# Kernel tuning notes

Hardware: AMD Instinct MI355X
Metric: run time of the kernel (lower is better)

The kernel has to match this reference:

```python
import jax, jax.numpy as jnp
import numpy as np

B = 128          # batch
DIM_CODES = 256  # codes per sample
EMB = 16         # embedding dim per code
BOOK = 1024      # codebook entries per code position
Z = 512          # latent dim
NPSEUDO = 16     # pseudo inputs (VampPrior)
WDIM = DIM_CODES * EMB  # 4096


def setup_inputs() -> dict:
    key = jax.random.key(0)
    k0, k1, k2, k3, k4 = jax.random.split(key, 5)
    s = 0.02
    return {
        "w_q": jax.random.normal(k0, (B, WDIM), jnp.float32),
        "pseudo_inputs": jax.random.normal(k1, (NPSEUDO, EMB, DIM_CODES), jnp.float32),
        "W_enc": jax.random.normal(k2, (EMB * DIM_CODES, 2 * Z), jnp.float32) * s,
        "b_enc": jnp.zeros((2 * Z,), jnp.float32),
        "W_dec": jax.random.normal(k3, (Z, WDIM), jnp.float32) * s,
        "b_dec": jnp.zeros((WDIM,), jnp.float32),
        "codebook": jax.random.normal(k4, (DIM_CODES, BOOK, EMB), jnp.float32),
    }


def _dist(w_recon, codebook):
    # pykeops_square_distance: per-code squared L2 distance to all book entries
    x = w_recon.reshape(-1, DIM_CODES, EMB)              # (B, dc, e)
    x2 = jnp.sum(x * x, axis=-1)                         # (B, dc)
    c2 = jnp.sum(codebook * codebook, axis=-1)           # (dc, book)
    cross = jnp.einsum('bde,dke->bdk', x, codebook)      # (B, dc, book)
    d = x2[:, :, None] - 2.0 * cross + c2[None, :, :]    # (B, dc, book)
    idx = jnp.argmin(d, axis=2)[..., None]               # (B, dc, 1)
    return d, idx


def reference(w_q, pseudo_inputs, W_enc, b_enc, W_dec, b_dec, codebook):
    # encode: reshape w_q to (B, emb, dim_codes), append pseudo inputs
    x = jnp.swapaxes(w_q.reshape(-1, DIM_CODES, EMB), 1, 2)   # (B, e, dc)
    x = jnp.concatenate([x, pseudo_inputs], axis=0)           # (B+P, e, dc)
    h = x.reshape(x.shape[0], -1) @ W_enc + b_enc             # (B+P, 2Z)
    batch = h[:-NPSEUDO]                                      # drop pseudo rows
    mu, log_var = jnp.split(batch, 2, axis=1)                 # (B, Z) each
    z = mu                                                    # eval mode: gaussian_sample returns mu
    # decode
    w_recon = z @ W_dec + b_dec                               # (B, WDIM)
    cb = jax.lax.stop_gradient(codebook)                      # codebook.detach()
    w_dist, idx = _dist(w_recon, cb)
    return (w_dist, idx, w_recon, mu, log_var)
```

## Files before the change

### kernel.cpp

```cpp
#include <hip/hip_runtime.h>

#define OFF_WDIST 0
#define OFF_IDX   33554432
#define OFF_WREC  33587200
#define OFF_MU    34111488
#define OFF_LV    34177024

__device__ __forceinline__ float dot16(const float4* a, const float4* b) {
    float s = 0.f;
#pragma unroll
    for (int i = 0; i < 4; ++i) {
        s = fmaf(a[i].x, b[i].x, s);
        s = fmaf(a[i].y, b[i].y, s);
        s = fmaf(a[i].z, b[i].z, s);
        s = fmaf(a[i].w, b[i].w, s);
    }
    return s;
}

__global__ __launch_bounds__(256) void enc_gemm1_kernel(const float* __restrict__ w_q,
                                                        const float* __restrict__ W_enc,
                                                        float* __restrict__ part) {
    __shared__ float xs_t[64 * 128];
    __shared__ float ws[64 * 128];
    const int tid = threadIdx.x;
    const int jt = blockIdx.x & 7;
    const int kc = blockIdx.x >> 3;

    {
        const int b = tid >> 1;
        const int half = tid & 1;
        const float* src = w_q + b * 4096 + kc * 64;
#pragma unroll
        for (int u = 0; u < 8; ++u) {
            const int l0 = half * 32 + u * 4;
            const float4 v = *(const float4*)(src + l0);
            xs_t[(l0 + 0) * 128 + b] = v.x;
            xs_t[(l0 + 1) * 128 + b] = v.y;
            xs_t[(l0 + 2) * 128 + b] = v.z;
            xs_t[(l0 + 3) * 128 + b] = v.w;
        }
    }
    {
        const int l = tid >> 2;
        const int q = tid & 3;
        const int gi = (l & 15) * 256 + kc * 4 + (l >> 4);
        const float* src = W_enc + (size_t)gi * 1024 + jt * 128 + q * 32;
        float* dst = &ws[l * 128 + q * 32];
#pragma unroll
        for (int u = 0; u < 8; ++u) {
            *(float4*)(dst + u * 4) = *(const float4*)(src + u * 4);
        }
    }
    __syncthreads();

    const int tx = tid & 15;
    const int ty = tid >> 4;
    float acc[8][8];
#pragma unroll
    for (int r = 0; r < 8; ++r)
#pragma unroll
        for (int c = 0; c < 8; ++c) acc[r][c] = 0.f;

    for (int l = 0; l < 64; ++l) {
        const float4 a0 = *(const float4*)&xs_t[l * 128 + ty * 8];
        const float4 a1 = *(const float4*)&xs_t[l * 128 + ty * 8 + 4];
        const float4 w0 = *(const float4*)&ws[l * 128 + tx * 4];
        const float4 w1 = *(const float4*)&ws[l * 128 + 64 + tx * 4];
        const float av[8] = {a0.x, a0.y, a0.z, a0.w, a1.x, a1.y, a1.z, a1.w};
        const float wv[8] = {w0.x, w0.y, w0.z, w0.w, w1.x, w1.y, w1.z, w1.w};
#pragma unroll
        for (int r = 0; r < 8; ++r)
#pragma unroll
            for (int c = 0; c < 8; ++c)
                acc[r][c] = fmaf(av[r], wv[c], acc[r][c]);
    }

#pragma unroll
    for (int r = 0; r < 8; ++r) {
        const int brow = ty * 8 + r;
        float* dst = part + (size_t)(kc * 128 + brow) * 1024 + jt * 128;
        *(float4*)(dst + tx * 4)      = make_float4(acc[r][0], acc[r][1], acc[r][2], acc[r][3]);
        *(float4*)(dst + 64 + tx * 4) = make_float4(acc[r][4], acc[r][5], acc[r][6], acc[r][7]);
    }
}

__global__ __launch_bounds__(256) void enc_reduce_kernel(const float* __restrict__ part,
                                                         const float* __restrict__ b_enc,
                                                         float* __restrict__ mu_out,
                                                         float* __restrict__ lv_out) {
    const int g = blockIdx.x * 256 + threadIdx.x;
    const int b = g >> 10;
    const int j = g & 1023;
    float sum = b_enc[j];
#pragma unroll 8
    for (int kc = 0; kc < 64; ++kc) {
        sum += part[(size_t)((kc * 128 + b) << 10) + j];
    }
    if (j < 512) mu_out[b * 512 + j] = sum;
    else         lv_out[b * 512 + (j - 512)] = sum;
}

__global__ __launch_bounds__(256) void dec_gemm1_kernel(const float* __restrict__ mu_in,
                                                        const float* __restrict__ W_dec,
                                                        float* __restrict__ part) {
    __shared__ float xs_t[32 * 128];
    __shared__ float ws[32 * 128];
    const int tid = threadIdx.x;
    const int ct = blockIdx.x & 31;
    const int kc = blockIdx.x >> 5;

    {
        const int b = tid >> 1;
        const int half = tid & 1;
        const float* src = mu_in + b * 512 + kc * 32;
#pragma unroll
        for (int u = 0; u < 4; ++u) {
            const int l0 = half * 16 + u * 4;
            const float4 v = *(const float4*)(src + l0);
            xs_t[(l0 + 0) * 128 + b] = v.x;
            xs_t[(l0 + 1) * 128 + b] = v.y;
            xs_t[(l0 + 2) * 128 + b] = v.z;
            xs_t[(l0 + 3) * 128 + b] = v.w;
        }
    }
    {
        const int l = tid >> 3;
        const int q = tid & 7;
        const float* src = W_dec + (size_t)(kc * 32 + l) * 4096 + ct * 128 + q * 16;
        float* dst = &ws[l * 128 + q * 16];
#pragma unroll
        for (int u = 0; u < 4; ++u) {
            *(float4*)(dst + u * 4) = *(const float4*)(src + u * 4);
        }
    }
    __syncthreads();

    const int tx = tid & 15;
    const int ty = tid >> 4;
    float acc[8][8];
#pragma unroll
    for (int r = 0; r < 8; ++r)
#pragma unroll
        for (int c = 0; c < 8; ++c) acc[r][c] = 0.f;

    for (int l = 0; l < 32; ++l) {
        const float4 a0 = *(const float4*)&xs_t[l * 128 + ty * 8];
        const float4 a1 = *(const float4*)&xs_t[l * 128 + ty * 8 + 4];
        const float4 w0 = *(const float4*)&ws[l * 128 + tx * 4];
        const float4 w1 = *(const float4*)&ws[l * 128 + 64 + tx * 4];
        const float av[8] = {a0.x, a0.y, a0.z, a0.w, a1.x, a1.y, a1.z, a1.w};
        const float wv[8] = {w0.x, w0.y, w0.z, w0.w, w1.x, w1.y, w1.z, w1.w};
#pragma unroll
        for (int r = 0; r < 8; ++r)
#pragma unroll
            for (int c = 0; c < 8; ++c)
                acc[r][c] = fmaf(av[r], wv[c], acc[r][c]);
    }

#pragma unroll
    for (int r = 0; r < 8; ++r) {
        const int brow = ty * 8 + r;
        float* dst = part + (size_t)(kc * 128 + brow) * 4096 + ct * 128;
        *(float4*)(dst + tx * 4)      = make_float4(acc[r][0], acc[r][1], acc[r][2], acc[r][3]);
        *(float4*)(dst + 64 + tx * 4) = make_float4(acc[r][4], acc[r][5], acc[r][6], acc[r][7]);
    }
}

__global__ __launch_bounds__(256) void dec_reduce_kernel(const float* __restrict__ part,
                                                         const float* __restrict__ b_dec,
                                                         float* __restrict__ wrec_out) {
    const int g = blockIdx.x * 256 + threadIdx.x;
    const int b = g >> 12;
    const int n = g & 4095;
    float sum = b_dec[n];
#pragma unroll
    for (int kc = 0; kc < 16; ++kc) {
        sum += part[(size_t)((kc * 128 + b) << 12) + n];
    }
    wrec_out[b * 4096 + n] = sum;
}

__global__ __launch_bounds__(256) void dist_kernel(const float* __restrict__ wrec,
                                                   const float* __restrict__ cbk,
                                                   float* __restrict__ wdist,
                                                   float* __restrict__ idx_out) {
    const int dc = blockIdx.x & 255;
    const int bg = blockIdx.x >> 8;
    const int t = threadIdx.x;

    float4 xr[8][4];
    float x2[8];
#pragma unroll
    for (int r = 0; r < 8; ++r) {
        const float4* p = (const float4*)(wrec + (bg * 8 + r) * 4096 + dc * 16);
        xr[r][0] = p[0]; xr[r][1] = p[1]; xr[r][2] = p[2]; xr[r][3] = p[3];
        x2[r] = dot16(xr[r], xr[r]);
    }

    const float* cbp = cbk + (size_t)dc * 1024 * 16;
    float dv[8][4];
    float minv[8];
    int mink[8];
#pragma unroll
    for (int r = 0; r < 8; ++r) { minv[r] = 3.4e38f; mink[r] = 0; }

    const int k0 = t * 4;
#pragma unroll
    for (int kk = 0; kk < 4; ++kk) {
        const int k = k0 + kk;
        const float4* cp = (const float4*)(cbp + (size_t)k * 16);
        float4 cv[4];
        cv[0] = cp[0]; cv[1] = cp[1]; cv[2] = cp[2]; cv[3] = cp[3];
        const float cc = dot16(cv, cv);
#pragma unroll
        for (int r = 0; r < 8; ++r) {
            const float cr = dot16(xr[r], cv);
            const float dd = (x2[r] - 2.f * cr) + cc;
            dv[r][kk] = dd;
            if (dd < minv[r]) { minv[r] = dd; mink[r] = k; }
        }
    }

#pragma unroll
    for (int r = 0; r < 8; ++r) {
        float4 o = make_float4(dv[r][0], dv[r][1], dv[r][2], dv[r][3]);
        *(float4*)(wdist + (size_t)((bg * 8 + r) * 256 + dc) * 1024 + k0) = o;
    }

    __shared__ float rvs[8][4];
    __shared__ int rks[8][4];
    const int lane = t & 63;
    const int wv = t >> 6;
#pragma unroll
    for (int r = 0; r < 8; ++r) {
        float v = minv[r];
        int k = mink[r];
#pragma unroll
        for (int off = 32; off > 0; off >>= 1) {
            float ov = __shfl_down(v, off);
            int ok = __shfl_down(k, off);
            if (ov < v || (ov == v && ok < k)) { v = ov; k = ok; }
        }
        if (lane == 0) { rvs[r][wv] = v; rks[r][wv] = k; }
    }
    __syncthreads();
    if (t < 8) {
        float v = rvs[t][0];
        int k = rks[t][0];
#pragma unroll
        for (int w = 1; w < 4; ++w) {
            float ov = rvs[t][w];
            int ok = rks[t][w];
            if (ov < v || (ov == v && ok < k)) { v = ov; k = ok; }
        }
        idx_out[(bg * 8 + t) * 256 + dc] = (float)k;
    }
}

extern "C" void kernel_launch(void* const* d_in, const int* in_sizes, int n_in,
                              void* d_out, int out_size, void* d_ws, size_t ws_size,
                              hipStream_t stream) {
    const float* w_q   = (const float*)d_in[0];
    const float* W_enc = (const float*)d_in[2];
    const float* b_enc = (const float*)d_in[3];
    const float* W_dec = (const float*)d_in[4];
    const float* b_dec = (const float*)d_in[5];
    const float* cbk   = (const float*)d_in[6];
    float* out = (float*)d_out;

    float* mu_out = out + OFF_MU;
    float* lv_out = out + OFF_LV;
    float* wrec   = out + OFF_WREC;
    float* wdist  = out + OFF_WDIST;
    float* idx_o  = out + OFF_IDX;
    float* part   = out + OFF_WDIST;

    hipLaunchKernelGGL(enc_gemm1_kernel,  dim3(512),  dim3(256), 0, stream, w_q, W_enc, part);
    hipLaunchKernelGGL(enc_reduce_kernel, dim3(512),  dim3(256), 0, stream, part, b_enc, mu_out, lv_out);
    hipLaunchKernelGGL(dec_gemm1_kernel,  dim3(512),  dim3(256), 0, stream, mu_out, W_dec, part);
    hipLaunchKernelGGL(dec_reduce_kernel, dim3(2048), dim3(256), 0, stream, part, b_dec, wrec);
    hipLaunchKernelGGL(dist_kernel,       dim3(4096), dim3(256), 0, stream, wrec, cbk, wdist, idx_o);
}
```

Baseline: 260.0 us.

## Stream weights from global in GEMMs, halve column tiles, restructure distance kernel

Both encoder and decoder split-K GEMMs stop staging weights in shared memory. Each thread now reads its float4 of weights straight from global memory, with a narrower 64-column tile per block and twice as many blocks. The distance kernel moves the 8 query rows into shared memory and gives each thread a strided set of codebook entries, so every lane writes one float per row coalesced instead of a float4. The aims are to cut LDS traffic and register pressure and to raise occupancy. The cost is more global/L2 weight reads and more scalar stores.

```diff
diff --git a/kernel.cpp b/kernel.cpp
--- a/kernel.cpp
+++ b/kernel.cpp
@@ -6,82 +6,68 @@
 #define OFF_MU    34111488
 #define OFF_LV    34177024
 
-__device__ __forceinline__ float dot16(const float4* a, const float4* b) {
-    float s = 0.f;
-#pragma unroll
-    for (int i = 0; i < 4; ++i) {
-        s = fmaf(a[i].x, b[i].x, s);
-        s = fmaf(a[i].y, b[i].y, s);
-        s = fmaf(a[i].z, b[i].z, s);
-        s = fmaf(a[i].w, b[i].w, s);
-    }
-    return s;
-}
-
 __global__ __launch_bounds__(256) void enc_gemm1_kernel(const float* __restrict__ w_q,
                                                         const float* __restrict__ W_enc,
                                                         float* __restrict__ part) {
     __shared__ float xs_t[64 * 128];
-    __shared__ float ws[64 * 128];
     const int tid = threadIdx.x;
-    const int jt = blockIdx.x & 7;
-    const int kc = blockIdx.x >> 3;
+    const int jt = blockIdx.x & 15;
+    const int kc = blockIdx.x >> 4;
 
     {
-        const int b = tid >> 1;
-        const int half = tid & 1;
-        const float* src = w_q + b * 4096 + kc * 64;
-#pragma unroll
-        for (int u = 0; u < 8; ++u) {
-            const int l0 = half * 32 + u * 4;
-            const float4 v = *(const float4*)(src + l0);
-            xs_t[(l0 + 0) * 128 + b] = v.x;
-            xs_t[(l0 + 1) * 128 + b] = v.y;
-            xs_t[(l0 + 2) * 128 + b] = v.z;
-            xs_t[(l0 + 3) * 128 + b] = v.w;
-        }
-    }
-    {
-        const int l = tid >> 2;
+        const int b0 = tid >> 2;
         const int q = tid & 3;
-        const int gi = (l & 15) * 256 + kc * 4 + (l >> 4);
-        const float* src = W_enc + (size_t)gi * 1024 + jt * 128 + q * 32;
-        float* dst = &ws[l * 128 + q * 32];
-#pragma unroll
-        for (int u = 0; u < 8; ++u) {
-            *(float4*)(dst + u * 4) = *(const float4*)(src + u * 4);
+#pragma unroll
+        for (int pass = 0; pass < 2; ++pass) {
+            const int b = pass * 64 + b0;
+            const float* src = w_q + b * 4096 + kc * 64 + q * 16;
+#pragma unroll
+            for (int u = 0; u < 4; ++u) {
+                const float4 v = *(const float4*)(src + u * 4);
+                const int l0 = q * 16 + u * 4;
+                xs_t[(l0 + 0) * 128 + b] = v.x;
+                xs_t[(l0 + 1) * 128 + b] = v.y;
+                xs_t[(l0 + 2) * 128 + b] = v.z;
+                xs_t[(l0 + 3) * 128 + b] = v.w;
+            }
         }
     }
     __syncthreads();
 
     const int tx = tid & 15;
     const int ty = tid >> 4;
-    float acc[8][8];
+    const float* wp = W_enc + (size_t)(kc * 4) * 1024 + jt * 64 + tx * 4;
+
+    float acc[8][4];
 #pragma unroll
     for (int r = 0; r < 8; ++r)
 #pragma unroll
-        for (int c = 0; c < 8; ++c) acc[r][c] = 0.f;
-
-    for (int l = 0; l < 64; ++l) {
-        const float4 a0 = *(const float4*)&xs_t[l * 128 + ty * 8];
-        const float4 a1 = *(const float4*)&xs_t[l * 128 + ty * 8 + 4];
-        const float4 w0 = *(const float4*)&ws[l * 128 + tx * 4];
-        const float4 w1 = *(const float4*)&ws[l * 128 + 64 + tx * 4];
-        const float av[8] = {a0.x, a0.y, a0.z, a0.w, a1.x, a1.y, a1.z, a1.w};
-        const float wv[8] = {w0.x, w0.y, w0.z, w0.w, w1.x, w1.y, w1.z, w1.w};
-#pragma unroll
-        for (int r = 0; r < 8; ++r)
-#pragma unroll
-            for (int c = 0; c < 8; ++c)
-                acc[r][c] = fmaf(av[r], wv[c], acc[r][c]);
+        for (int c = 0; c < 4; ++c) acc[r][c] = 0.f;
+
+#pragma unroll 2
+    for (int e = 0; e < 16; ++e) {
+#pragma unroll
+        for (int d = 0; d < 4; ++d) {
+            const float4 w = *(const float4*)(wp + (size_t)(e * 256 + d) * 1024);
+            const int l = d * 16 + e;
+            const float4 a0 = *(const float4*)&xs_t[l * 128 + ty * 8];
+            const float4 a1 = *(const float4*)&xs_t[l * 128 + ty * 8 + 4];
+            const float av[8] = {a0.x, a0.y, a0.z, a0.w, a1.x, a1.y, a1.z, a1.w};
+#pragma unroll
+            for (int r = 0; r < 8; ++r) {
+                acc[r][0] = fmaf(av[r], w.x, acc[r][0]);
+                acc[r][1] = fmaf(av[r], w.y, acc[r][1]);
+                acc[r][2] = fmaf(av[r], w.z, acc[r][2]);
+                acc[r][3] = fmaf(av[r], w.w, acc[r][3]);
+            }
+        }
     }
 
 #pragma unroll
     for (int r = 0; r < 8; ++r) {
         const int brow = ty * 8 + r;
-        float* dst = part + (size_t)(kc * 128 + brow) * 1024 + jt * 128;
-        *(float4*)(dst + tx * 4)      = make_float4(acc[r][0], acc[r][1], acc[r][2], acc[r][3]);
-        *(float4*)(dst + 64 + tx * 4) = make_float4(acc[r][4], acc[r][5], acc[r][6], acc[r][7]);
+        float* dst = part + (size_t)(kc * 128 + brow) * 1024 + jt * 64 + tx * 4;
+        *(float4*)dst = make_float4(acc[r][0], acc[r][1], acc[r][2], acc[r][3]);
     }
 }
 
@@ -105,65 +91,56 @@
                                                         const float* __restrict__ W_dec,
                                                         float* __restrict__ part) {
     __shared__ float xs_t[32 * 128];
-    __shared__ float ws[32 * 128];
     const int tid = threadIdx.x;
-    const int ct = blockIdx.x & 31;
-    const int kc = blockIdx.x >> 5;
+    const int ct = blockIdx.x & 63;
+    const int kc = blockIdx.x >> 6;
 
     {
         const int b = tid >> 1;
-        const int half = tid & 1;
-        const float* src = mu_in + b * 512 + kc * 32;
+        const int q = tid & 1;
+        const float* src = mu_in + b * 512 + kc * 32 + q * 16;
 #pragma unroll
         for (int u = 0; u < 4; ++u) {
-            const int l0 = half * 16 + u * 4;
-            const float4 v = *(const float4*)(src + l0);
+            const float4 v = *(const float4*)(src + u * 4);
+            const int l0 = q * 16 + u * 4;
             xs_t[(l0 + 0) * 128 + b] = v.x;
             xs_t[(l0 + 1) * 128 + b] = v.y;
             xs_t[(l0 + 2) * 128 + b] = v.z;
             xs_t[(l0 + 3) * 128 + b] = v.w;
         }
     }
-    {
-        const int l = tid >> 3;
-        const int q = tid & 7;
-        const float* src = W_dec + (size_t)(kc * 32 + l) * 4096 + ct * 128 + q * 16;
-        float* dst = &ws[l * 128 + q * 16];
-#pragma unroll
-        for (int u = 0; u < 4; ++u) {
-            *(float4*)(dst + u * 4) = *(const float4*)(src + u * 4);
-        }
-    }
     __syncthreads();
 
     const int tx = tid & 15;
     const int ty = tid >> 4;
-    float acc[8][8];
+    const float* wp = W_dec + (size_t)(kc * 32) * 4096 + ct * 64 + tx * 4;
+
+    float acc[8][4];
 #pragma unroll
     for (int r = 0; r < 8; ++r)
 #pragma unroll
-        for (int c = 0; c < 8; ++c) acc[r][c] = 0.f;
-
+        for (int c = 0; c < 4; ++c) acc[r][c] = 0.f;
+
+#pragma unroll 8
     for (int l = 0; l < 32; ++l) {
+        const float4 w = *(const float4*)(wp + (size_t)l * 4096);
         const float4 a0 = *(const float4*)&xs_t[l * 128 + ty * 8];
         const float4 a1 = *(const float4*)&xs_t[l * 128 + ty * 8 + 4];
-        const float4 w0 = *(const float4*)&ws[l * 128 + tx * 4];
-        const float4 w1 = *(const float4*)&ws[l * 128 + 64 + tx * 4];
         const float av[8] = {a0.x, a0.y, a0.z, a0.w, a1.x, a1.y, a1.z, a1.w};
-        const float wv[8] = {w0.x, w0.y, w0.z, w0.w, w1.x, w1.y, w1.z, w1.w};
-#pragma unroll
-        for (int r = 0; r < 8; ++r)
-#pragma unroll
-            for (int c = 0; c < 8; ++c)
-                acc[r][c] = fmaf(av[r], wv[c], acc[r][c]);
+#pragma unroll
+        for (int r = 0; r < 8; ++r) {
+            acc[r][0] = fmaf(av[r], w.x, acc[r][0]);
+            acc[r][1] = fmaf(av[r], w.y, acc[r][1]);
+            acc[r][2] = fmaf(av[r], w.z, acc[r][2]);
+            acc[r][3] = fmaf(av[r], w.w, acc[r][3]);
+        }
     }
 
 #pragma unroll
     for (int r = 0; r < 8; ++r) {
         const int brow = ty * 8 + r;
-        float* dst = part + (size_t)(kc * 128 + brow) * 4096 + ct * 128;
-        *(float4*)(dst + tx * 4)      = make_float4(acc[r][0], acc[r][1], acc[r][2], acc[r][3]);
-        *(float4*)(dst + 64 + tx * 4) = make_float4(acc[r][4], acc[r][5], acc[r][6], acc[r][7]);
+        float* dst = part + (size_t)(kc * 128 + brow) * 4096 + ct * 64 + tx * 4;
+        *(float4*)dst = make_float4(acc[r][0], acc[r][1], acc[r][2], acc[r][3]);
     }
 }
 
@@ -189,43 +166,63 @@
     const int bg = blockIdx.x >> 8;
     const int t = threadIdx.x;
 
-    float4 xr[8][4];
-    float x2[8];
-#pragma unroll
-    for (int r = 0; r < 8; ++r) {
-        const float4* p = (const float4*)(wrec + (bg * 8 + r) * 4096 + dc * 16);
-        xr[r][0] = p[0]; xr[r][1] = p[1]; xr[r][2] = p[2]; xr[r][3] = p[3];
-        x2[r] = dot16(xr[r], xr[r]);
-    }
-
-    const float* cbp = cbk + (size_t)dc * 1024 * 16;
-    float dv[8][4];
+    __shared__ float xs[8][16];
+    __shared__ float x2s[8];
+
+    if (t < 32) {
+        const int r = t >> 2, q = t & 3;
+        *(float4*)&xs[r][q * 4] =
+            *(const float4*)(wrec + (size_t)(bg * 8 + r) * 4096 + dc * 16 + q * 4);
+    }
+    __syncthreads();
+    if (t < 8) {
+        float s = 0.f;
+#pragma unroll
+        for (int i = 0; i < 16; ++i) s = fmaf(xs[t][i], xs[t][i], s);
+        x2s[t] = s;
+    }
+    __syncthreads();
+
+    const float* cbp = cbk + (size_t)dc * 16384;
     float minv[8];
     int mink[8];
 #pragma unroll
     for (int r = 0; r < 8; ++r) { minv[r] = 3.4e38f; mink[r] = 0; }
 
-    const int k0 = t * 4;
-#pragma unroll
     for (int kk = 0; kk < 4; ++kk) {
-        const int k = k0 + kk;
+        const int k = kk * 256 + t;
         const float4* cp = (const float4*)(cbp + (size_t)k * 16);
-        float4 cv[4];
-        cv[0] = cp[0]; cv[1] = cp[1]; cv[2] = cp[2]; cv[3] = cp[3];
-        const float cc = dot16(cv, cv);
+        const float4 c0 = cp[0], c1 = cp[1], c2 = cp[2], c3 = cp[3];
+        float cc = 0.f;
+        cc = fmaf(c0.x, c0.x, cc); cc = fmaf(c0.y, c0.y, cc);
+        cc = fmaf(c0.z, c0.z, cc); cc = fmaf(c0.w, c0.w, cc);
+        cc = fmaf(c1.x, c1.x, cc); cc = fmaf(c1.y, c1.y, cc);
+        cc = fmaf(c1.z, c1.z, cc); cc = fmaf(c1.w, c1.w, cc);
+        cc = fmaf(c2.x, c2.x, cc); cc = fmaf(c2.y, c2.y, cc);
+        cc = fmaf(c2.z, c2.z, cc); cc = fmaf(c2.w, c2.w, cc);
+        cc = fmaf(c3.x, c3.x, cc); cc = fmaf(c3.y, c3.y, cc);
+        cc = fmaf(c3.z, c3.z, cc); cc = fmaf(c3.w, c3.w, cc);
+
+        float* obase = wdist + (size_t)((bg * 8) * 256 + dc) * 1024 + k;
 #pragma unroll
         for (int r = 0; r < 8; ++r) {
-            const float cr = dot16(xr[r], cv);
-            const float dd = (x2[r] - 2.f * cr) + cc;
-            dv[r][kk] = dd;
+            const float4 x0 = *(const float4*)&xs[r][0];
+            const float4 x1 = *(const float4*)&xs[r][4];
+            const float4 x2v = *(const float4*)&xs[r][8];
+            const float4 x3 = *(const float4*)&xs[r][12];
+            float cr = 0.f;
+            cr = fmaf(x0.x, c0.x, cr); cr = fmaf(x0.y, c0.y, cr);
+            cr = fmaf(x0.z, c0.z, cr); cr = fmaf(x0.w, c0.w, cr);
+            cr = fmaf(x1.x, c1.x, cr); cr = fmaf(x1.y, c1.y, cr);
+            cr = fmaf(x1.z, c1.z, cr); cr = fmaf(x1.w, c1.w, cr);
+            cr = fmaf(x2v.x, c2.x, cr); cr = fmaf(x2v.y, c2.y, cr);
+            cr = fmaf(x2v.z, c2.z, cr); cr = fmaf(x2v.w, c2.w, cr);
+            cr = fmaf(x3.x, c3.x, cr); cr = fmaf(x3.y, c3.y, cr);
+            cr = fmaf(x3.z, c3.z, cr); cr = fmaf(x3.w, c3.w, cr);
+            const float dd = (x2s[r] + cc) - 2.f * cr;
+            obase[(size_t)r * 262144] = dd;
             if (dd < minv[r]) { minv[r] = dd; mink[r] = k; }
         }
-    }
-
-#pragma unroll
-    for (int r = 0; r < 8; ++r) {
-        float4 o = make_float4(dv[r][0], dv[r][1], dv[r][2], dv[r][3]);
-        *(float4*)(wdist + (size_t)((bg * 8 + r) * 256 + dc) * 1024 + k0) = o;
     }
 
     __shared__ float rvs[8][4];
@@ -276,9 +273,9 @@
     float* idx_o  = out + OFF_IDX;
     float* part   = out + OFF_WDIST;
 
-    hipLaunchKernelGGL(enc_gemm1_kernel,  dim3(512),  dim3(256), 0, stream, w_q, W_enc, part);
+    hipLaunchKernelGGL(enc_gemm1_kernel,  dim3(1024), dim3(256), 0, stream, w_q, W_enc, part);
     hipLaunchKernelGGL(enc_reduce_kernel, dim3(512),  dim3(256), 0, stream, part, b_enc, mu_out, lv_out);
-    hipLaunchKernelGGL(dec_gemm1_kernel,  dim3(512),  dim3(256), 0, stream, mu_out, W_dec, part);
+    hipLaunchKernelGGL(dec_gemm1_kernel,  dim3(1024), dim3(256), 0, stream, mu_out, W_dec, part);
     hipLaunchKernelGGL(dec_reduce_kernel, dim3(2048), dim3(256), 0, stream, part, b_dec, wrec);
     hipLaunchKernelGGL(dist_kernel,       dim3(4096), dim3(256), 0, stream, wrec, cbk, wdist, idx_o);
 }
```

New measurement: 290.1 us. 11.6% more time.
